# Performance work log

Measured on AMD Instinct MI355X. Metric: run time of the kernel, lower is better.

Reference implementation:

```python
import jax, jax.numpy as jnp
import numpy as np

QMAX = 127.0  # int8 symmetric
EPS = 1e-8


def _fake_quant(v, scale):
    # quantize/clamp/dequantize with straight-through rounding (STE clip)
    s = jnp.maximum(scale, EPS)
    scaled = v / s
    clipped = jnp.clip(scaled, -QMAX, QMAX)
    q = clipped + jax.lax.stop_gradient(jnp.round(clipped) - clipped)
    return q * s


def setup_inputs() -> dict:
    key = jax.random.key(0)
    kx, kw, kb = jax.random.split(key, 3)
    B, S, D_IN, D_OUT = 8, 2048, 4096, 4096
    x = jax.random.normal(kx, (B, S, D_IN), dtype=jnp.float32)
    weight = jax.random.normal(kw, (D_OUT, D_IN), dtype=jnp.float32) * 0.02
    bias = jax.random.normal(kb, (D_OUT,), dtype=jnp.float32) * 0.02
    return {"x": x, "weight": weight, "bias": bias}


def reference(x, weight, bias):
    # activation: dynamic per-tensor symmetric int8 fake-quant
    a_scale = jnp.max(jnp.abs(x)) / QMAX
    xq = _fake_quant(x, a_scale)
    # weight: per-channel (output-channel axis 0) symmetric int8 fake-quant
    w_scale = jnp.max(jnp.abs(weight), axis=1, keepdims=True) / QMAX  # [out, 1]
    wq = _fake_quant(weight, w_scale)
    # F.linear: y = x @ W^T + b
    return jnp.einsum('bsd,od->bso', xq, wq) + bias
```

## Files before the change

### kernel.cpp

```cpp
#include <hip/hip_runtime.h>
#include <hip/hip_bf16.h>
#include <stdint.h>


#define QMAX_F 127.0f
#define EPS_F 1e-8f

typedef int v4i __attribute__((ext_vector_type(4)));

static constexpr size_t WSCALE_OFF = 64;
static constexpr size_t XQ_OFF = 1u << 16;

__global__ void absmax_kernel(const float4* __restrict__ x, unsigned* __restrict__ out, int n4) {
    int tid = blockIdx.x * blockDim.x + threadIdx.x;
    int stride = gridDim.x * blockDim.x;
    float m = 0.0f;
    for (int i = tid; i < n4; i += stride) {
        float4 v = x[i];
        m = fmaxf(m, fmaxf(fmaxf(fabsf(v.x), fabsf(v.y)), fmaxf(fabsf(v.z), fabsf(v.w))));
    }
    for (int off = 32; off > 0; off >>= 1)
        m = fmaxf(m, __shfl_xor(m, off));
    __shared__ float wmax[4];
    int lane = threadIdx.x & 63, wid = threadIdx.x >> 6;
    if (lane == 0) wmax[wid] = m;
    __syncthreads();
    if (threadIdx.x == 0) {
        float b = fmaxf(fmaxf(wmax[0], wmax[1]), fmaxf(wmax[2], wmax[3]));
        atomicMax(out, __float_as_uint(b));
    }
}

__device__ __forceinline__ int quant1(float v, float s) {
    float t = v / s;
    t = fminf(fmaxf(t, -QMAX_F), QMAX_F);
    return (int)rintf(t);
}

__global__ void quantx_kernel(const float4* __restrict__ x, const unsigned* __restrict__ amax,
                              int* __restrict__ xq, int n4) {
    float s = fmaxf(__uint_as_float(*amax) / QMAX_F, EPS_F);
    int tid = blockIdx.x * blockDim.x + threadIdx.x;
    int stride = gridDim.x * blockDim.x;
    for (int i = tid; i < n4; i += stride) {
        float4 v = x[i];
        int q0 = quant1(v.x, s), q1 = quant1(v.y, s), q2 = quant1(v.z, s), q3 = quant1(v.w, s);
        xq[i] = (q0 & 0xff) | ((q1 & 0xff) << 8) | ((q2 & 0xff) << 16) | ((q3 & 0xff) << 24);
    }
}

__global__ void quantw_kernel(const float4* __restrict__ w, int* __restrict__ wq,
                              float* __restrict__ w_scale, int K4) {
    int row = blockIdx.x;
    const float4* wr = w + (size_t)row * K4;
    int t = threadIdx.x;
    float4 vals[4];
    float m = 0.0f;
    for (int i = 0; i < 4; i++) {
        float4 v = wr[t + 256 * i];
        vals[i] = v;
        m = fmaxf(m, fmaxf(fmaxf(fabsf(v.x), fabsf(v.y)), fmaxf(fabsf(v.z), fabsf(v.w))));
    }
    for (int off = 32; off > 0; off >>= 1)
        m = fmaxf(m, __shfl_xor(m, off));
    __shared__ float sm[4];
    if ((t & 63) == 0) sm[t >> 6] = m;
    __syncthreads();
    float mb = fmaxf(fmaxf(sm[0], sm[1]), fmaxf(sm[2], sm[3]));
    float s = fmaxf(mb / QMAX_F, EPS_F);
    if (t == 0) w_scale[row] = s;
    int* wqr = wq + (size_t)row * K4;
    for (int i = 0; i < 4; i++) {
        float4 v = vals[i];
        int q0 = quant1(v.x, s), q1 = quant1(v.y, s), q2 = quant1(v.z, s), q3 = quant1(v.w, s);
        wqr[t + 256 * i] = (q0 & 0xff) | ((q1 & 0xff) << 8) | ((q2 & 0xff) << 16) | ((q3 & 0xff) << 24);
    }
}

#define BM 256
#define BN 256
#define BKB 128

__device__ __forceinline__ void gload16(const char* g, char* l) {
    __builtin_amdgcn_global_load_lds(
        (const __attribute__((address_space(1))) void*)g,
        (__attribute__((address_space(3))) void*)l, 16, 0, 0);
}

__global__ __launch_bounds__(512, 2) void gemm_i8_8ph(
    const char* __restrict__ xq, const char* __restrict__ wq,
    const float* __restrict__ w_scale, const unsigned* __restrict__ amax,
    const float* __restrict__ bias, float* __restrict__ out,
    int M, int N, int K) {
    __shared__ __align__(16) char lds[131072];

    const int nwg = gridDim.x, bid = blockIdx.x;
    const int cpx = nwg >> 3;
    const int swz = (bid & 7) * cpx + (bid >> 3);
    const int nbm = M / BM;
    const int bm = swz % nbm, bn = swz / nbm;

    const int t = threadIdx.x;
    const int lane = t & 63, wid = t >> 6;
    const int wr = wid >> 2, wc = wid & 3;

    const int srow = t >> 3;
    const int scol = ((t & 7) ^ (srow & 7)) << 4;
    const char* aSrc = xq + (size_t)(bm * BM + srow) * K + scol;
    const char* bSrc = wq + (size_t)(bn * BN + srow) * K + scol;
    char* ldsT = lds + t * 16;

    auto stageA = [&](int half, int tt, int ktc) {
        char* d = ldsT + ((unsigned)(tt & 1) << 16) + ((unsigned)half << 14);
        gload16(aSrc + (size_t)(half * 128) * K + ktc, d);
        gload16(aSrc + (size_t)(half * 128 + 64) * K + ktc, d + 8192);
    };
    auto stageB = [&](int half, int tt, int ktc) {
        char* d = ldsT + ((unsigned)(tt & 1) << 16) + 32768u + ((unsigned)half << 14);
        gload16(bSrc + (size_t)(half * 128) * K + ktc, d);
        gload16(bSrc + (size_t)(half * 128 + 64) * K + ktc, d + 8192);
    };

    const int rA = lane & 15, kg = lane >> 4, sw7 = lane & 7;
    const unsigned cks0 = (unsigned)((kg ^ sw7) << 4);
    const unsigned cks1 = (unsigned)(((4 + kg) ^ sw7) << 4);
    const unsigned aBase = ((unsigned)wr << 14) + ((unsigned)rA << 7);
    const unsigned bBase = 32768u + ((unsigned)wc << 13) + ((unsigned)rA << 7);

    v4i acc[8][4];
#pragma unroll
    for (int m = 0; m < 8; m++)
#pragma unroll
        for (int n = 0; n < 4; n++) acc[m][n] = (v4i){0, 0, 0, 0};

    const int nkt = K / BKB;

    stageA(0, 0, 0); stageA(1, 0, 0); stageB(0, 0, 0); stageB(1, 0, 0);
    {
        const int k1 = (1 < nkt) ? BKB : 0;
        stageB(0, 1, k1); stageA(0, 1, k1); stageB(1, 1, k1);
    }
    asm volatile("s_waitcnt vmcnt(6)" ::: "memory");
    __builtin_amdgcn_s_barrier();

    for (int T = 0; T < nkt; ++T) {
        const unsigned bb = (unsigned)(T & 1) << 16;
        const int kA1 = (T + 1 < nkt) ? (T + 1) * BKB : 0;
        const int kT2 = (T + 2 < nkt) ? (T + 2) * BKB : 0;
        v4i a[4][2], b0[2][2], b1[2][2];

#pragma unroll
        for (int m = 0; m < 4; m++) {
            a[m][0] = *(const v4i*)(lds + bb + aBase + ((unsigned)m << 11) + cks0);
            a[m][1] = *(const v4i*)(lds + bb + aBase + ((unsigned)m << 11) + cks1);
        }
#pragma unroll
        for (int n = 0; n < 2; n++) {
            b0[n][0] = *(const v4i*)(lds + bb + bBase + ((unsigned)n << 11) + cks0);
            b0[n][1] = *(const v4i*)(lds + bb + bBase + ((unsigned)n << 11) + cks1);
        }
        stageA(1, T + 1, kA1);
        __builtin_amdgcn_s_barrier();
        asm volatile("s_waitcnt lgkmcnt(0)" ::: "memory");
        __builtin_amdgcn_sched_barrier(0);
        __builtin_amdgcn_s_setprio(1);
#pragma unroll
        for (int ks = 0; ks < 2; ks++)
#pragma unroll
            for (int m = 0; m < 4; m++)
#pragma unroll
                for (int n = 0; n < 2; n++)
                    acc[m][n] = __builtin_amdgcn_mfma_i32_16x16x64_i8(a[m][ks], b0[n][ks], acc[m][n], 0, 0, 0);
        __builtin_amdgcn_s_setprio(0);
        __builtin_amdgcn_s_barrier();

#pragma unroll
        for (int n = 0; n < 2; n++) {
            b1[n][0] = *(const v4i*)(lds + bb + bBase + 4096u + ((unsigned)n << 11) + cks0);
            b1[n][1] = *(const v4i*)(lds + bb + bBase + 4096u + ((unsigned)n << 11) + cks1);
        }
        __builtin_amdgcn_s_barrier();
        asm volatile("s_waitcnt lgkmcnt(0)" ::: "memory");
        __builtin_amdgcn_sched_barrier(0);
        __builtin_amdgcn_s_setprio(1);
#pragma unroll
        for (int ks = 0; ks < 2; ks++)
#pragma unroll
            for (int m = 0; m < 4; m++)
#pragma unroll
                for (int n = 0; n < 2; n++)
                    acc[m][2 + n] = __builtin_amdgcn_mfma_i32_16x16x64_i8(a[m][ks], b1[n][ks], acc[m][2 + n], 0, 0, 0);
        __builtin_amdgcn_s_setprio(0);
        __builtin_amdgcn_s_barrier();

#pragma unroll
        for (int m = 0; m < 4; m++) {
            a[m][0] = *(const v4i*)(lds + bb + aBase + 8192u + ((unsigned)m << 11) + cks0);
            a[m][1] = *(const v4i*)(lds + bb + aBase + 8192u + ((unsigned)m << 11) + cks1);
        }
        stageB(0, T + 2, kT2);
        __builtin_amdgcn_s_barrier();
        asm volatile("s_waitcnt lgkmcnt(0)" ::: "memory");
        __builtin_amdgcn_sched_barrier(0);
        __builtin_amdgcn_s_setprio(1);
#pragma unroll
        for (int ks = 0; ks < 2; ks++)
#pragma unroll
            for (int m = 0; m < 4; m++)
#pragma unroll
                for (int n = 0; n < 2; n++)
                    acc[4 + m][2 + n] = __builtin_amdgcn_mfma_i32_16x16x64_i8(a[m][ks], b1[n][ks], acc[4 + m][2 + n], 0, 0, 0);
        __builtin_amdgcn_s_setprio(0);
        __builtin_amdgcn_s_barrier();

        stageA(0, T + 2, kT2);
        stageB(1, T + 2, kT2);
        asm volatile("s_waitcnt vmcnt(6)" ::: "memory");
        __builtin_amdgcn_s_barrier();
        __builtin_amdgcn_s_setprio(1);
#pragma unroll
        for (int ks = 0; ks < 2; ks++)
#pragma unroll
            for (int m = 0; m < 4; m++)
#pragma unroll
                for (int n = 0; n < 2; n++)
                    acc[4 + m][n] = __builtin_amdgcn_mfma_i32_16x16x64_i8(a[m][ks], b0[n][ks], acc[4 + m][n], 0, 0, 0);
        __builtin_amdgcn_s_setprio(0);
        __builtin_amdgcn_s_barrier();
    }

    float a_s = fmaxf(__uint_as_float(*amax) / QMAX_F, EPS_F);
    const int row0 = bm * BM + wr * 128 + (kg << 2);
    const int col0 = bn * BN + wc * 64 + rA;
#pragma unroll
    for (int n = 0; n < 4; n++) {
        int col = col0 + n * 16;
        float f = a_s * w_scale[col];
        float bv = bias[col];
#pragma unroll
        for (int m = 0; m < 8; m++) {
            size_t base = (size_t)(row0 + m * 16) * N + col;
#pragma unroll
            for (int j = 0; j < 4; j++)
                out[base + (size_t)j * N] = (float)acc[m][n][j] * f + bv;
        }
    }
}

extern "C" void kernel_launch(void* const* d_in, const int* in_sizes, int n_in,
                              void* d_out, int out_size, void* d_ws, size_t ws_size,
                              hipStream_t stream) {
    const float* x = (const float*)d_in[0];
    const float* w = (const float*)d_in[1];
    const float* bias = (const float*)d_in[2];
    float* out = (float*)d_out;

    const int N = in_sizes[2];
    const int K = in_sizes[1] / N;
    const int M = in_sizes[0] / K;

    char* ws = (char*)d_ws;
    unsigned* amax = (unsigned*)ws;
    float* w_scale = (float*)(ws + WSCALE_OFF);
    char* xq = ws + XQ_OFF;
    char* wq = ws + XQ_OFF + (size_t)M * K;

    size_t needed = XQ_OFF + (size_t)M * K + (size_t)N * K;
    if (ws_size < needed) return;

    hipMemsetAsync(amax, 0, 4, stream);

    int n4x = (M * K) / 4;
    absmax_kernel<<<2048, 256, 0, stream>>>((const float4*)x, amax, n4x);
    quantx_kernel<<<2048, 256, 0, stream>>>((const float4*)x, amax, (int*)xq, n4x);
    quantw_kernel<<<N, 256, 0, stream>>>((const float4*)w, (int*)wq, w_scale, K / 4);

    int grid = (M / BM) * (N / BN);
    gemm_i8_8ph<<<grid, 512, 0, stream>>>(xq, wq, w_scale, amax, bias, out, M, N, K);
}
```

Before: 445.7 us.

## Switch int8 GEMM to 32x32x32 MFMA and stage epilogue through LDS

```diff
diff --git a/kernel.cpp b/kernel.cpp
--- a/kernel.cpp
+++ b/kernel.cpp
@@ -7,6 +7,7 @@
 #define EPS_F 1e-8f
 
 typedef int v4i __attribute__((ext_vector_type(4)));
+typedef int v16i __attribute__((ext_vector_type(16)));
 
 static constexpr size_t WSCALE_OFF = 64;
 static constexpr size_t XQ_OFF = 1u << 16;
@@ -121,17 +122,20 @@
         gload16(bSrc + (size_t)(half * 128 + 64) * K + ktc, d + 8192);
     };
 
-    const int rA = lane & 15, kg = lane >> 4, sw7 = lane & 7;
-    const unsigned cks0 = (unsigned)((kg ^ sw7) << 4);
-    const unsigned cks1 = (unsigned)(((4 + kg) ^ sw7) << 4);
-    const unsigned aBase = ((unsigned)wr << 14) + ((unsigned)rA << 7);
-    const unsigned bBase = 32768u + ((unsigned)wc << 13) + ((unsigned)rA << 7);
-
-    v4i acc[8][4];
-#pragma unroll
-    for (int m = 0; m < 8; m++)
-#pragma unroll
-        for (int n = 0; n < 4; n++) acc[m][n] = (v4i){0, 0, 0, 0};
+    const int r32 = lane & 31, kh = lane >> 5, sw7 = r32 & 7;
+    unsigned cks[4];
+#pragma unroll
+    for (int ks = 0; ks < 4; ks++) cks[ks] = (unsigned)(((2 * ks + kh) ^ sw7) << 4);
+    const unsigned aB = ((unsigned)wr << 14) + ((unsigned)r32 << 7);
+    const unsigned bB = 32768u + ((unsigned)wc << 13) + ((unsigned)r32 << 7);
+
+    v16i acc[4][2];
+#pragma unroll
+    for (int mi = 0; mi < 4; mi++)
+#pragma unroll
+        for (int ni = 0; ni < 2; ni++)
+#pragma unroll
+            for (int r = 0; r < 16; r++) acc[mi][ni][r] = 0;
 
     const int nkt = K / BKB;
 
@@ -147,69 +151,59 @@
         const unsigned bb = (unsigned)(T & 1) << 16;
         const int kA1 = (T + 1 < nkt) ? (T + 1) * BKB : 0;
         const int kT2 = (T + 2 < nkt) ? (T + 2) * BKB : 0;
-        v4i a[4][2], b0[2][2], b1[2][2];
-
-#pragma unroll
-        for (int m = 0; m < 4; m++) {
-            a[m][0] = *(const v4i*)(lds + bb + aBase + ((unsigned)m << 11) + cks0);
-            a[m][1] = *(const v4i*)(lds + bb + aBase + ((unsigned)m << 11) + cks1);
-        }
-#pragma unroll
-        for (int n = 0; n < 2; n++) {
-            b0[n][0] = *(const v4i*)(lds + bb + bBase + ((unsigned)n << 11) + cks0);
-            b0[n][1] = *(const v4i*)(lds + bb + bBase + ((unsigned)n << 11) + cks1);
-        }
+        v4i a[2][4], b0[4], b1[4];
+
+#pragma unroll
+        for (int mi = 0; mi < 2; mi++)
+#pragma unroll
+            for (int ks = 0; ks < 4; ks++)
+                a[mi][ks] = *(const v4i*)(lds + bb + aB + ((unsigned)mi << 12) + cks[ks]);
+#pragma unroll
+        for (int ks = 0; ks < 4; ks++)
+            b0[ks] = *(const v4i*)(lds + bb + bB + cks[ks]);
         stageA(1, T + 1, kA1);
         __builtin_amdgcn_s_barrier();
         asm volatile("s_waitcnt lgkmcnt(0)" ::: "memory");
         __builtin_amdgcn_sched_barrier(0);
         __builtin_amdgcn_s_setprio(1);
 #pragma unroll
-        for (int ks = 0; ks < 2; ks++)
-#pragma unroll
-            for (int m = 0; m < 4; m++)
-#pragma unroll
-                for (int n = 0; n < 2; n++)
-                    acc[m][n] = __builtin_amdgcn_mfma_i32_16x16x64_i8(a[m][ks], b0[n][ks], acc[m][n], 0, 0, 0);
-        __builtin_amdgcn_s_setprio(0);
-        __builtin_amdgcn_s_barrier();
-
-#pragma unroll
-        for (int n = 0; n < 2; n++) {
-            b1[n][0] = *(const v4i*)(lds + bb + bBase + 4096u + ((unsigned)n << 11) + cks0);
-            b1[n][1] = *(const v4i*)(lds + bb + bBase + 4096u + ((unsigned)n << 11) + cks1);
-        }
+        for (int ks = 0; ks < 4; ks++)
+#pragma unroll
+            for (int mi = 0; mi < 2; mi++)
+                acc[mi][0] = __builtin_amdgcn_mfma_i32_32x32x32_i8(a[mi][ks], b0[ks], acc[mi][0], 0, 0, 0);
+        __builtin_amdgcn_s_setprio(0);
+        __builtin_amdgcn_s_barrier();
+
+#pragma unroll
+        for (int ks = 0; ks < 4; ks++)
+            b1[ks] = *(const v4i*)(lds + bb + bB + 4096u + cks[ks]);
         __builtin_amdgcn_s_barrier();
         asm volatile("s_waitcnt lgkmcnt(0)" ::: "memory");
         __builtin_amdgcn_sched_barrier(0);
         __builtin_amdgcn_s_setprio(1);
 #pragma unroll
-        for (int ks = 0; ks < 2; ks++)
-#pragma unroll
-            for (int m = 0; m < 4; m++)
-#pragma unroll
-                for (int n = 0; n < 2; n++)
-                    acc[m][2 + n] = __builtin_amdgcn_mfma_i32_16x16x64_i8(a[m][ks], b1[n][ks], acc[m][2 + n], 0, 0, 0);
-        __builtin_amdgcn_s_setprio(0);
-        __builtin_amdgcn_s_barrier();
-
-#pragma unroll
-        for (int m = 0; m < 4; m++) {
-            a[m][0] = *(const v4i*)(lds + bb + aBase + 8192u + ((unsigned)m << 11) + cks0);
-            a[m][1] = *(const v4i*)(lds + bb + aBase + 8192u + ((unsigned)m << 11) + cks1);
-        }
+        for (int ks = 0; ks < 4; ks++)
+#pragma unroll
+            for (int mi = 0; mi < 2; mi++)
+                acc[mi][1] = __builtin_amdgcn_mfma_i32_32x32x32_i8(a[mi][ks], b1[ks], acc[mi][1], 0, 0, 0);
+        __builtin_amdgcn_s_setprio(0);
+        __builtin_amdgcn_s_barrier();
+
+#pragma unroll
+        for (int mi = 0; mi < 2; mi++)
+#pragma unroll
+            for (int ks = 0; ks < 4; ks++)
+                a[mi][ks] = *(const v4i*)(lds + bb + aB + 8192u + ((unsigned)mi << 12) + cks[ks]);
         stageB(0, T + 2, kT2);
         __builtin_amdgcn_s_barrier();
         asm volatile("s_waitcnt lgkmcnt(0)" ::: "memory");
         __builtin_amdgcn_sched_barrier(0);
         __builtin_amdgcn_s_setprio(1);
 #pragma unroll
-        for (int ks = 0; ks < 2; ks++)
-#pragma unroll
-            for (int m = 0; m < 4; m++)
-#pragma unroll
-                for (int n = 0; n < 2; n++)
-                    acc[4 + m][2 + n] = __builtin_amdgcn_mfma_i32_16x16x64_i8(a[m][ks], b1[n][ks], acc[4 + m][2 + n], 0, 0, 0);
+        for (int ks = 0; ks < 4; ks++)
+#pragma unroll
+            for (int mi = 0; mi < 2; mi++)
+                acc[2 + mi][1] = __builtin_amdgcn_mfma_i32_32x32x32_i8(a[mi][ks], b1[ks], acc[2 + mi][1], 0, 0, 0);
         __builtin_amdgcn_s_setprio(0);
         __builtin_amdgcn_s_barrier();
 
@@ -219,30 +213,41 @@
         __builtin_amdgcn_s_barrier();
         __builtin_amdgcn_s_setprio(1);
 #pragma unroll
-        for (int ks = 0; ks < 2; ks++)
-#pragma unroll
-            for (int m = 0; m < 4; m++)
-#pragma unroll
-                for (int n = 0; n < 2; n++)
-                    acc[4 + m][n] = __builtin_amdgcn_mfma_i32_16x16x64_i8(a[m][ks], b0[n][ks], acc[4 + m][n], 0, 0, 0);
-        __builtin_amdgcn_s_setprio(0);
-        __builtin_amdgcn_s_barrier();
-    }
-
-    float a_s = fmaxf(__uint_as_float(*amax) / QMAX_F, EPS_F);
-    const int row0 = bm * BM + wr * 128 + (kg << 2);
-    const int col0 = bn * BN + wc * 64 + rA;
-#pragma unroll
-    for (int n = 0; n < 4; n++) {
-        int col = col0 + n * 16;
-        float f = a_s * w_scale[col];
-        float bv = bias[col];
-#pragma unroll
-        for (int m = 0; m < 8; m++) {
-            size_t base = (size_t)(row0 + m * 16) * N + col;
-#pragma unroll
-            for (int j = 0; j < 4; j++)
-                out[base + (size_t)j * N] = (float)acc[m][n][j] * f + bv;
+        for (int ks = 0; ks < 4; ks++)
+#pragma unroll
+            for (int mi = 0; mi < 2; mi++)
+                acc[2 + mi][0] = __builtin_amdgcn_mfma_i32_32x32x32_i8(a[mi][ks], b0[ks], acc[2 + mi][0], 0, 0, 0);
+        __builtin_amdgcn_s_setprio(0);
+        __builtin_amdgcn_s_barrier();
+    }
+
+    float* ldsF = (float*)lds;
+    const float a_s = fmaxf(__uint_as_float(*amax) / QMAX_F, EPS_F);
+    const int col0 = bn * BN + wc * 64 + r32;
+    const float f0 = a_s * w_scale[col0], f1 = a_s * w_scale[col0 + 32];
+    const float bv0 = bias[col0], bv1 = bias[col0 + 32];
+    const unsigned wcol0 = (unsigned)(wc * 64 + r32);
+
+#pragma unroll
+    for (int round = 0; round < 2; ++round) {
+        __syncthreads();
+        if (wr == round) {
+#pragma unroll
+            for (int mi = 0; mi < 4; mi++)
+#pragma unroll
+                for (int r = 0; r < 16; r++) {
+                    unsigned row = (unsigned)(mi * 32 + (r & 3) + 8 * (r >> 2) + 4 * kh);
+                    ldsF[row * 256 + wcol0] = (float)acc[mi][0][r] * f0 + bv0;
+                    ldsF[row * 256 + wcol0 + 32] = (float)acc[mi][1][r] * f1 + bv1;
+                }
+        }
+        __syncthreads();
+        const size_t gbase = (size_t)(bm * BM + round * 128) * N + bn * BN + lane * 4;
+#pragma unroll
+        for (int i = 0; i < 16; i++) {
+            int row = wid + 8 * i;
+            float4 v = *(const float4*)(ldsF + (unsigned)row * 256 + (unsigned)lane * 4);
+            *(float4*)(out + gbase + (size_t)row * N) = v;
         }
     }
 }
```

Result: slower. 478.1 us (+7.3%).
